# Performance work log

Hardware: AMD Instinct MI355X
Metric: run time of the kernel (lower is better)

## Reference

```python
import jax, jax.numpy as jnp
import numpy as np

DIM = 1024
N = 65536

def _l2norm(x):
    # F.normalize: x / max(||x||_2, eps) along last dim, eps=1e-12
    n = jnp.linalg.norm(x, axis=-1, keepdims=True)
    return x / jnp.maximum(n, 1e-12)

def setup_inputs() -> dict:
    key = jax.random.key(0)
    ks = jax.random.split(key, 10)
    s = 0.02
    return {
        "q_init": jax.random.normal(ks[0], (1, DIM), jnp.float32),
        "k_init": jax.random.normal(ks[1], (N, DIM), jnp.float32),
        "Wq": jax.random.normal(ks[2], (DIM, DIM // 2), jnp.float32) * s,
        "bq": jnp.zeros((DIM // 2,), jnp.float32),
        "Wk": jax.random.normal(ks[3], (DIM, DIM // 2), jnp.float32) * s,
        "bk": jnp.zeros((DIM // 2,), jnp.float32),
        "Wv": jax.random.normal(ks[4], (DIM, DIM), jnp.float32) * s,
        "bv": jnp.zeros((DIM,), jnp.float32),
        "Wm": jax.random.normal(ks[5], (DIM, DIM), jnp.float32) * s,
        "bm": jnp.zeros((DIM,), jnp.float32),
        "gamma": jnp.ones((1,), jnp.float32),
    }

def reference(q_init, k_init, Wq, bq, Wk, bk, Wv, bv, Wm, bm, gamma):
    q = _l2norm(q_init) @ Wq + bq              # [1, dim/2]
    kn = _l2norm(k_init)                        # [N, dim]
    k = kn @ Wk + bk                            # [N, dim/2]
    v = kn @ Wv + bv                            # [N, dim]
    scores = q @ k.T                            # [1, N]
    # global mean/std rescale (torch.std is unbiased, ddof=1)
    scores = (scores - scores.mean()) / (jnp.std(scores, ddof=1) + 1e-8)
    attn = jax.nn.softmax(jnp.clip(scores, -10.0, 10.0), axis=-1)
    # dropout is identity in eval mode
    out = (attn @ v) @ Wm + bm                  # [1, dim]
    g = jax.nn.sigmoid(gamma)                   # [1]
    return g * q_init + (1.0 - g) * out
```

## Files before the change

kernel.cpp:

```cpp
#include <hip/hip_runtime.h>
#include <math.h>

#define DIM   1024
#define HALF  512
#define NROWS 65536
#define SBLK  4096
#define WBLK  1024

#define OFF_QACC   0
#define OFF_PVEC   (OFF_QACC + HALF)
#define OFF_PSTAT  (OFF_PVEC + DIM)
#define OFF_S      (OFF_PSTAT + 2*SBLK)
#define OFF_INVN   (OFF_S + NROWS)
#define OFF_COEFF  (OFF_INVN + NROWS)
#define OFF_ESUM   (OFF_COEFF + NROWS)
#define OFF_PW     (OFF_ESUM + 256)
#define OFF_WACC   (OFF_PW + WBLK*DIM)
#define OFF_OVACC  (OFF_WACC + DIM)
#define OFF_END    (OFF_OVACC + DIM)

__global__ void k_q(const float* __restrict__ q_init,
                    const float* __restrict__ Wq,
                    float* __restrict__ qacc) {
    __shared__ float  shA[256];
    __shared__ float4 sh4[256];
    int t = threadIdx.x, b = blockIdx.x;
    float v0 = q_init[t], v1 = q_init[t + 256],
          v2 = q_init[t + 512], v3 = q_init[t + 768];
    shA[t] = v0 * v0 + v1 * v1 + v2 * v2 + v3 * v3;
    __syncthreads();
    for (int s = 128; s > 0; s >>= 1) {
        if (t < s) shA[t] += shA[t + s];
        __syncthreads();
    }
    float qinv = 1.0f / fmaxf(sqrtf(shA[0]), 1e-12f);
    const float4* W4 = (const float4*)Wq;
    float vv0 = v0 * qinv, vv1 = v1 * qinv, vv2 = v2 * qinv, vv3 = v3 * qinv;
    float4 m0 = W4[(size_t)t * (HALF / 4) + b];
    float4 m1 = W4[(size_t)(t + 256) * (HALF / 4) + b];
    float4 m2 = W4[(size_t)(t + 512) * (HALF / 4) + b];
    float4 m3 = W4[(size_t)(t + 768) * (HALF / 4) + b];
    float4 acc;
    acc.x = vv0 * m0.x + vv1 * m1.x + vv2 * m2.x + vv3 * m3.x;
    acc.y = vv0 * m0.y + vv1 * m1.y + vv2 * m2.y + vv3 * m3.y;
    acc.z = vv0 * m0.z + vv1 * m1.z + vv2 * m2.z + vv3 * m3.z;
    acc.w = vv0 * m0.w + vv1 * m1.w + vv2 * m2.w + vv3 * m3.w;
    sh4[t] = acc;
    __syncthreads();
    for (int s = 128; s > 0; s >>= 1) {
        if (t < s) {
            sh4[t].x += sh4[t + s].x; sh4[t].y += sh4[t + s].y;
            sh4[t].z += sh4[t + s].z; sh4[t].w += sh4[t + s].w;
        }
        __syncthreads();
    }
    if (t == 0) ((float4*)qacc)[b] = sh4[0];
}

__global__ void k_pvec(const float* __restrict__ Wk,
                       const float* __restrict__ qacc,
                       const float* __restrict__ bq,
                       float* __restrict__ pvec) {
    __shared__ float q[HALF];
    int t = threadIdx.x;
    for (int j = t; j < HALF; j += 256) q[j] = qacc[j] + bq[j];
    __syncthreads();
    int wave = t >> 6, lane = t & 63;
    int d = blockIdx.x * 4 + wave;
    const float* row = Wk + (size_t)d * HALF;
    float acc = 0.f;
    #pragma unroll
    for (int j0 = 0; j0 < HALF; j0 += 64) acc += row[j0 + lane] * q[j0 + lane];
    #pragma unroll
    for (int o = 32; o > 0; o >>= 1) acc += __shfl_down(acc, o);
    if (lane == 0) pvec[d] = acc;
}

__global__ void k_scores(const float* __restrict__ K,
                         const float* __restrict__ pvec,
                         float* __restrict__ svals,
                         float* __restrict__ invn,
                         float2* __restrict__ pstat) {
    __shared__ float4 p4s[256];
    __shared__ float wsum[4], wssq[4];
    int t = threadIdx.x;
    p4s[t] = ((const float4*)pvec)[t];
    __syncthreads();
    int wave = t >> 6, lane = t & 63;
    int row0 = blockIdx.x * 16 + wave * 4;
    const float4* k4 = (const float4*)K + (size_t)row0 * 256;
    float d0 = 0, d1 = 0, d2 = 0, d3 = 0;
    float q0 = 0, q1 = 0, q2 = 0, q3 = 0;
    #pragma unroll
    for (int i = 0; i < 4; ++i) {
        int idx = lane + i * 64;
        float4 p = p4s[idx];
        float4 a = k4[idx];
        float4 b = k4[256 + idx];
        float4 c = k4[512 + idx];
        float4 e = k4[768 + idx];
        d0 += a.x * p.x + a.y * p.y + a.z * p.z + a.w * p.w;
        q0 += a.x * a.x + a.y * a.y + a.z * a.z + a.w * a.w;
        d1 += b.x * p.x + b.y * p.y + b.z * p.z + b.w * p.w;
        q1 += b.x * b.x + b.y * b.y + b.z * b.z + b.w * b.w;
        d2 += c.x * p.x + c.y * p.y + c.z * p.z + c.w * p.w;
        q2 += c.x * c.x + c.y * c.y + c.z * c.z + c.w * c.w;
        d3 += e.x * p.x + e.y * p.y + e.z * p.z + e.w * p.w;
        q3 += e.x * e.x + e.y * e.y + e.z * e.z + e.w * e.w;
    }
    #pragma unroll
    for (int o = 32; o > 0; o >>= 1) {
        d0 += __shfl_down(d0, o); q0 += __shfl_down(q0, o);
        d1 += __shfl_down(d1, o); q1 += __shfl_down(q1, o);
        d2 += __shfl_down(d2, o); q2 += __shfl_down(q2, o);
        d3 += __shfl_down(d3, o); q3 += __shfl_down(q3, o);
    }
    if (lane == 0) {
        float i0 = 1.0f / fmaxf(sqrtf(q0), 1e-12f);
        float i1 = 1.0f / fmaxf(sqrtf(q1), 1e-12f);
        float i2 = 1.0f / fmaxf(sqrtf(q2), 1e-12f);
        float i3 = 1.0f / fmaxf(sqrtf(q3), 1e-12f);
        float s0 = d0 * i0, s1 = d1 * i1, s2 = d2 * i2, s3 = d3 * i3;
        float4 sv = make_float4(s0, s1, s2, s3);
        float4 iv = make_float4(i0, i1, i2, i3);
        *(float4*)(svals + row0) = sv;
        *(float4*)(invn + row0) = iv;
        wsum[wave] = s0 + s1 + s2 + s3;
        wssq[wave] = s0 * s0 + s1 * s1 + s2 * s2 + s3 * s3;
    }
    __syncthreads();
    if (t == 0)
        pstat[blockIdx.x] = make_float2(wsum[0] + wsum[1] + wsum[2] + wsum[3],
                                        wssq[0] + wssq[1] + wssq[2] + wssq[3]);
}

__global__ void k_coeff2(const float* __restrict__ svals,
                         const float* __restrict__ invn,
                         const float2* __restrict__ pstat,
                         float* __restrict__ coeff,
                         float* __restrict__ esum) {
    __shared__ float rs[256], rq[256];
    int t = threadIdx.x, b = blockIdx.x;
    float s = 0.f, q = 0.f;
    for (int i = t; i < SBLK; i += 256) {
        float2 p = pstat[i];
        s += p.x; q += p.y;
    }
    rs[t] = s; rq[t] = q;
    __syncthreads();
    for (int k = 128; k > 0; k >>= 1) {
        if (t < k) { rs[t] += rs[t + k]; rq[t] += rq[t + k]; }
        __syncthreads();
    }
    float mean = rs[0] / (float)NROWS;
    float var  = (rq[0] - (float)NROWS * mean * mean) / (float)(NROWS - 1);
    float rstd = 1.0f / (sqrtf(fmaxf(var, 0.0f)) + 1e-8f);
    int i = b * 256 + t;
    float z = (svals[i] - mean) * rstd;
    z = fminf(fmaxf(z, -10.0f), 10.0f);
    float e = expf(z);
    coeff[i] = e * invn[i];
    __syncthreads();
    rs[t] = e;
    __syncthreads();
    for (int k = 128; k > 0; k >>= 1) {
        if (t < k) rs[t] += rs[t + k];
        __syncthreads();
    }
    if (t == 0) esum[b] = rs[0];
}

__global__ void k_wsum(const float* __restrict__ K,
                       const float* __restrict__ coeff,
                       float* __restrict__ pw) {
    int t = threadIdx.x;
    int r0 = blockIdx.x * 64;
    const float4* M4 = (const float4*)K + (size_t)r0 * 256 + t;
    const float* cf = coeff + r0;
    float4 acc = make_float4(0.f, 0.f, 0.f, 0.f);
    #pragma unroll 16
    for (int r = 0; r < 64; ++r) {
        float c = cf[r];
        float4 m = M4[(size_t)r * 256];
        acc.x += c * m.x; acc.y += c * m.y; acc.z += c * m.z; acc.w += c * m.w;
    }
    ((float4*)pw)[(size_t)blockIdx.x * 256 + t] = acc;
}

__global__ void k_wred(const float* __restrict__ pw,
                       const float* __restrict__ esum,
                       float* __restrict__ wacc) {
    __shared__ float  rs[256];
    __shared__ float4 sh4[256];
    int t = threadIdx.x, b = blockIdx.x;
    rs[t] = esum[t];
    __syncthreads();
    for (int k = 128; k > 0; k >>= 1) {
        if (t < k) rs[t] += rs[t + k];
        __syncthreads();
    }
    float inv = 1.0f / rs[0];
    const float4* pw4 = (const float4*)pw;
    int c4 = b * 64 + (t & 63);
    int qr = t >> 6;
    float4 acc = make_float4(0.f, 0.f, 0.f, 0.f);
    #pragma unroll 8
    for (int p = qr * 256; p < qr * 256 + 256; ++p) {
        float4 m = pw4[(size_t)p * 256 + c4];
        acc.x += m.x; acc.y += m.y; acc.z += m.z; acc.w += m.w;
    }
    sh4[t] = acc;
    __syncthreads();
    if (t < 64) {
        float4 a = sh4[t], b4 = sh4[t + 64], c = sh4[t + 128], d = sh4[t + 192];
        float4 w;
        w.x = (a.x + b4.x + c.x + d.x) * inv;
        w.y = (a.y + b4.y + c.y + d.y) * inv;
        w.z = (a.z + b4.z + c.z + d.z) * inv;
        w.w = (a.w + b4.w + c.w + d.w) * inv;
        ((float4*)wacc)[b * 64 + t] = w;
    }
}

__global__ void k_matvec_col(const float* __restrict__ M,
                             const float* __restrict__ coeff,
                             const float* __restrict__ cbias,
                             float* __restrict__ out,
                             int nrows, int ncols4) {
    __shared__ float4 red[256];
    int t = threadIdx.x, c4 = blockIdx.x;
    const float4* M4 = (const float4*)M;
    float4 acc = make_float4(0.f, 0.f, 0.f, 0.f);
    for (int r = t; r < nrows; r += 256) {
        float c = coeff[r];
        if (cbias) c += cbias[r];
        float4 m = M4[(size_t)r * ncols4 + c4];
        acc.x += c * m.x; acc.y += c * m.y; acc.z += c * m.z; acc.w += c * m.w;
    }
    red[t] = acc;
    __syncthreads();
    for (int s = 128; s > 0; s >>= 1) {
        if (t < s) {
            red[t].x += red[t + s].x; red[t].y += red[t + s].y;
            red[t].z += red[t + s].z; red[t].w += red[t + s].w;
        }
        __syncthreads();
    }
    if (t == 0) ((float4*)out)[c4] = red[0];
}

__global__ void k_mv_final(const float* __restrict__ Wm,
                           const float* __restrict__ ovacc,
                           const float* __restrict__ bv,
                           const float* __restrict__ q_init,
                           const float* __restrict__ bm,
                           const float* __restrict__ gamma,
                           float* __restrict__ out) {
    __shared__ float4 sh4[256];
    int t = threadIdx.x, b = blockIdx.x;
    const float4* W4 = (const float4*)Wm;
    float4 acc = make_float4(0.f, 0.f, 0.f, 0.f);
    for (int r = t; r < DIM; r += 256) {
        float c = ovacc[r] + bv[r];
        float4 m = W4[(size_t)r * 256 + b];
        acc.x += c * m.x; acc.y += c * m.y; acc.z += c * m.z; acc.w += c * m.w;
    }
    sh4[t] = acc;
    __syncthreads();
    for (int s = 128; s > 0; s >>= 1) {
        if (t < s) {
            sh4[t].x += sh4[t + s].x; sh4[t].y += sh4[t + s].y;
            sh4[t].z += sh4[t + s].z; sh4[t].w += sh4[t + s].w;
        }
        __syncthreads();
    }
    if (t == 0) {
        float g = 1.0f / (1.0f + expf(-gamma[0]));
        float4 o  = sh4[0];
        float4 qi = ((const float4*)q_init)[b];
        float4 bb = ((const float4*)bm)[b];
        float4 res;
        res.x = g * qi.x + (1.0f - g) * (o.x + bb.x);
        res.y = g * qi.y + (1.0f - g) * (o.y + bb.y);
        res.z = g * qi.z + (1.0f - g) * (o.z + bb.z);
        res.w = g * qi.w + (1.0f - g) * (o.w + bb.w);
        ((float4*)out)[b] = res;
    }
}

extern "C" void kernel_launch(void* const* d_in, const int* in_sizes, int n_in,
                              void* d_out, int out_size, void* d_ws, size_t ws_size,
                              hipStream_t stream) {
    const float* q_init = (const float*)d_in[0];
    const float* k_init = (const float*)d_in[1];
    const float* Wq     = (const float*)d_in[2];
    const float* bq     = (const float*)d_in[3];
    const float* Wk     = (const float*)d_in[4];
    const float* Wv     = (const float*)d_in[6];
    const float* bv     = (const float*)d_in[7];
    const float* Wm     = (const float*)d_in[8];
    const float* bm     = (const float*)d_in[9];
    const float* gamma  = (const float*)d_in[10];
    float* out = (float*)d_out;
    float* ws  = (float*)d_ws;

    float*  qacc   = ws + OFF_QACC;
    float*  pvec   = ws + OFF_PVEC;
    float2* pstat  = (float2*)(ws + OFF_PSTAT);
    float*  svals  = ws + OFF_S;
    float*  invn   = ws + OFF_INVN;
    float*  coeff  = ws + OFF_COEFF;
    float*  esum   = ws + OFF_ESUM;
    float*  pw     = ws + OFF_PW;
    float*  wacc   = ws + OFF_WACC;
    float*  ovacc  = ws + OFF_OVACC;

    k_q<<<HALF / 4, 256, 0, stream>>>(q_init, Wq, qacc);
    k_pvec<<<DIM / 4, 256, 0, stream>>>(Wk, qacc, bq, pvec);
    k_scores<<<SBLK, 256, 0, stream>>>(k_init, pvec, svals, invn, pstat);
    k_coeff2<<<NROWS / 256, 256, 0, stream>>>(svals, invn, pstat, coeff, esum);
    k_wsum<<<WBLK, 256, 0, stream>>>(k_init, coeff, pw);
    k_wred<<<4, 256, 0, stream>>>(pw, esum, wacc);
    k_matvec_col<<<DIM / 4, 256, 0, stream>>>(Wv, wacc, nullptr, ovacc, DIM, DIM / 4);
    k_mv_final<<<DIM / 4, 256, 0, stream>>>(Wm, ovacc, bv, q_init, bm, gamma, out);
}
```

Baseline: 477.1 us.

## Fuse softmax coefficient computation into weighted-sum kernel and widen final reduction

Merges the coefficient kernel into the weighted row-sum kernel. Each block now rebuilds the global mean and std from the partial stats and computes its own 64 exp coefficients in shared memory, which removes one launch and the coeff buffer round trip. The partial-sum reduction is spread over 32 blocks instead of 4 to get more parallelism. The cost is that every one of 1024 blocks re-reads the 4096 partial stats.

```diff
diff --git a/kernel.cpp b/kernel.cpp
--- a/kernel.cpp
+++ b/kernel.cpp
@@ -12,9 +12,8 @@
 #define OFF_PSTAT  (OFF_PVEC + DIM)
 #define OFF_S      (OFF_PSTAT + 2*SBLK)
 #define OFF_INVN   (OFF_S + NROWS)
-#define OFF_COEFF  (OFF_INVN + NROWS)
-#define OFF_ESUM   (OFF_COEFF + NROWS)
-#define OFF_PW     (OFF_ESUM + 256)
+#define OFF_ESUM   (OFF_INVN + NROWS)
+#define OFF_PW     (OFF_ESUM + WBLK)
 #define OFF_WACC   (OFF_PW + WBLK*DIM)
 #define OFF_OVACC  (OFF_WACC + DIM)
 #define OFF_END    (OFF_OVACC + DIM)
@@ -134,12 +133,14 @@
                                         wssq[0] + wssq[1] + wssq[2] + wssq[3]);
 }
 
-__global__ void k_coeff2(const float* __restrict__ svals,
-                         const float* __restrict__ invn,
-                         const float2* __restrict__ pstat,
-                         float* __restrict__ coeff,
-                         float* __restrict__ esum) {
+__global__ void k_wsumc(const float* __restrict__ K,
+                        const float* __restrict__ svals,
+                        const float* __restrict__ invn,
+                        const float2* __restrict__ pstat,
+                        float* __restrict__ pw,
+                        float* __restrict__ esum) {
     __shared__ float rs[256], rq[256];
+    __shared__ float cf[64];
     int t = threadIdx.x, b = blockIdx.x;
     float s = 0.f, q = 0.f;
     for (int i = t; i < SBLK; i += 256) {
@@ -155,28 +156,19 @@
     float mean = rs[0] / (float)NROWS;
     float var  = (rq[0] - (float)NROWS * mean * mean) / (float)(NROWS - 1);
     float rstd = 1.0f / (sqrtf(fmaxf(var, 0.0f)) + 1e-8f);
-    int i = b * 256 + t;
-    float z = (svals[i] - mean) * rstd;
-    z = fminf(fmaxf(z, -10.0f), 10.0f);
-    float e = expf(z);
-    coeff[i] = e * invn[i];
-    __syncthreads();
-    rs[t] = e;
-    __syncthreads();
-    for (int k = 128; k > 0; k >>= 1) {
-        if (t < k) rs[t] += rs[t + k];
-        __syncthreads();
-    }
-    if (t == 0) esum[b] = rs[0];
-}
-
-__global__ void k_wsum(const float* __restrict__ K,
-                       const float* __restrict__ coeff,
-                       float* __restrict__ pw) {
-    int t = threadIdx.x;
-    int r0 = blockIdx.x * 64;
+    int r0 = b * 64;
+    if (t < 64) {
+        float z = (svals[r0 + t] - mean) * rstd;
+        z = fminf(fmaxf(z, -10.0f), 10.0f);
+        float e = expf(z);
+        cf[t] = e * invn[r0 + t];
+        float es = e;
+        #pragma unroll
+        for (int o = 32; o > 0; o >>= 1) es += __shfl_down(es, o);
+        if (t == 0) esum[b] = es;
+    }
+    __syncthreads();
     const float4* M4 = (const float4*)K + (size_t)r0 * 256 + t;
-    const float* cf = coeff + r0;
     float4 acc = make_float4(0.f, 0.f, 0.f, 0.f);
     #pragma unroll 16
     for (int r = 0; r < 64; ++r) {
@@ -184,16 +176,19 @@
         float4 m = M4[(size_t)r * 256];
         acc.x += c * m.x; acc.y += c * m.y; acc.z += c * m.z; acc.w += c * m.w;
     }
-    ((float4*)pw)[(size_t)blockIdx.x * 256 + t] = acc;
-}
-
-__global__ void k_wred(const float* __restrict__ pw,
-                       const float* __restrict__ esum,
-                       float* __restrict__ wacc) {
+    ((float4*)pw)[(size_t)b * 256 + t] = acc;
+}
+
+__global__ void k_wred2(const float* __restrict__ pw,
+                        const float* __restrict__ esum,
+                        float* __restrict__ wacc) {
     __shared__ float  rs[256];
     __shared__ float4 sh4[256];
     int t = threadIdx.x, b = blockIdx.x;
-    rs[t] = esum[t];
+    float es = 0.f;
+    #pragma unroll
+    for (int i = 0; i < 4; ++i) es += esum[t + i * 256];
+    rs[t] = es;
     __syncthreads();
     for (int k = 128; k > 0; k >>= 1) {
         if (t < k) rs[t] += rs[t + k];
@@ -201,24 +196,27 @@
     }
     float inv = 1.0f / rs[0];
     const float4* pw4 = (const float4*)pw;
-    int c4 = b * 64 + (t & 63);
-    int qr = t >> 6;
+    int co = t & 7, rg = t >> 3;
+    int c4 = b * 8 + co;
     float4 acc = make_float4(0.f, 0.f, 0.f, 0.f);
     #pragma unroll 8
-    for (int p = qr * 256; p < qr * 256 + 256; ++p) {
-        float4 m = pw4[(size_t)p * 256 + c4];
+    for (int r = rg * 32; r < rg * 32 + 32; ++r) {
+        float4 m = pw4[(size_t)r * 256 + c4];
         acc.x += m.x; acc.y += m.y; acc.z += m.z; acc.w += m.w;
     }
     sh4[t] = acc;
     __syncthreads();
-    if (t < 64) {
-        float4 a = sh4[t], b4 = sh4[t + 64], c = sh4[t + 128], d = sh4[t + 192];
-        float4 w;
-        w.x = (a.x + b4.x + c.x + d.x) * inv;
-        w.y = (a.y + b4.y + c.y + d.y) * inv;
-        w.z = (a.z + b4.z + c.z + d.z) * inv;
-        w.w = (a.w + b4.w + c.w + d.w) * inv;
-        ((float4*)wacc)[b * 64 + t] = w;
+    for (int s = 16; s > 0; s >>= 1) {
+        if (rg < s) {
+            sh4[t].x += sh4[t + s * 8].x; sh4[t].y += sh4[t + s * 8].y;
+            sh4[t].z += sh4[t + s * 8].z; sh4[t].w += sh4[t + s * 8].w;
+        }
+        __syncthreads();
+    }
+    if (t < 8) {
+        float4 w = sh4[t];
+        ((float4*)wacc)[b * 8 + t] =
+            make_float4(w.x * inv, w.y * inv, w.z * inv, w.w * inv);
     }
 }
 
@@ -309,7 +307,6 @@
     float2* pstat  = (float2*)(ws + OFF_PSTAT);
     float*  svals  = ws + OFF_S;
     float*  invn   = ws + OFF_INVN;
-    float*  coeff  = ws + OFF_COEFF;
     float*  esum   = ws + OFF_ESUM;
     float*  pw     = ws + OFF_PW;
     float*  wacc   = ws + OFF_WACC;
@@ -318,9 +315,8 @@
     k_q<<<HALF / 4, 256, 0, stream>>>(q_init, Wq, qacc);
     k_pvec<<<DIM / 4, 256, 0, stream>>>(Wk, qacc, bq, pvec);
     k_scores<<<SBLK, 256, 0, stream>>>(k_init, pvec, svals, invn, pstat);
-    k_coeff2<<<NROWS / 256, 256, 0, stream>>>(svals, invn, pstat, coeff, esum);
-    k_wsum<<<WBLK, 256, 0, stream>>>(k_init, coeff, pw);
-    k_wred<<<4, 256, 0, stream>>>(pw, esum, wacc);
+    k_wsumc<<<WBLK, 256, 0, stream>>>(k_init, svals, invn, pstat, pw, esum);
+    k_wred2<<<32, 256, 0, stream>>>(pw, esum, wacc);
     k_matvec_col<<<DIM / 4, 256, 0, stream>>>(Wv, wacc, nullptr, ovacc, DIM, DIM / 4);
     k_mv_final<<<DIM / 4, 256, 0, stream>>>(Wm, ovacc, bv, q_init, bm, gamma, out);
 }
```

Result: faster. 454.3 us (-4.8%).
